# Kernel tuning notes

Hardware: AMD Instinct MI355X
Metric: run time of the kernel (lower is better)

The kernel has to match this reference:

```python
import jax, jax.numpy as jnp
import numpy as np

B, D, S = 8192, 512, 16
EPS = 1e-5


def setup_inputs() -> dict:
    key = jax.random.key(0)
    ks = jax.random.split(key, 12)
    w = lambda k, sh: (jax.random.normal(k, sh, dtype=jnp.float32) * 0.02)
    A_log = jnp.broadcast_to(jnp.log(jnp.arange(1, S + 1, dtype=jnp.float32)), (D, S))
    return {
        "x": jax.random.normal(ks[0], (B, D), dtype=jnp.float32),
        "ssm_state": jax.random.normal(ks[1], (B, D, S), dtype=jnp.float32) * 0.1,
        "ln_g": jnp.ones((D,), jnp.float32),
        "ln_b": jnp.zeros((D,), jnp.float32),
        "w1_W": w(ks[2], (D, D)), "w1_b": jnp.zeros((D,), jnp.float32),
        "v1_W": w(ks[3], (D, D)), "v1_b": jnp.zeros((D,), jnp.float32),
        "w2_W": w(ks[4], (D, D)), "w2_b": jnp.zeros((D,), jnp.float32),
        "conv_w": w(ks[5], (D, 1, 3)),  # depthwise Conv1d weight [C_out, 1, k]
        "A_log": A_log,
        "Bp_W": w(ks[6], (S, D)), "Bp_b": jnp.zeros((S,), jnp.float32),
        "Cp_W": w(ks[7], (S, D)), "Cp_b": jnp.zeros((S,), jnp.float32),
        "dt_W": w(ks[8], (D, D)), "dt_b": jnp.zeros((D,), jnp.float32),
    }


def reference(x, ssm_state, ln_g, ln_b, w1_W, w1_b, v1_W, v1_b, w2_W, w2_b,
              conv_w, A_log, Bp_W, Bp_b, Cp_W, Cp_b, dt_W, dt_b):
    # LayerNorm over d_model
    mu = jnp.mean(x, axis=-1, keepdims=True)
    var = jnp.mean(jnp.square(x - mu), axis=-1, keepdims=True)
    x_norm = (x - mu) * jax.lax.rsqrt(var + EPS) * ln_g + ln_b
    # w1 projection
    x1 = x_norm @ w1_W.T + w1_b
    # depthwise Conv1d on a length-1 sequence (unsqueeze(-1)): with k=3, pad=1,
    # zero padding means only the center tap contributes.
    x_conv = jax.nn.silu(x1 * conv_w[:, 0, 1])
    # selective-scan SSM single step (canonical Mamba recurrence)
    A = -jnp.exp(A_log)                                   # [D, S]
    delta = jax.nn.softplus(x_conv @ dt_W.T + dt_b)       # [B, D]
    Bm = x_conv @ Bp_W.T + Bp_b                           # [B, S]
    Cm = x_conv @ Cp_W.T + Cp_b                           # [B, S]
    dA = jnp.exp(delta[:, :, None] * A[None])             # [B, D, S]
    next_state = ssm_state * dA + (delta[:, :, None] * Bm[:, None, :]) * x_conv[:, :, None]
    x_ssm = jnp.sum(next_state * Cm[:, None, :], axis=-1)  # [B, D]
    # gate branch + output projection
    v = jax.nn.silu(x_norm @ v1_W.T + v1_b)
    out = (x_ssm * v) @ w2_W.T + w2_b
    return out, next_state
```

## Files before the change

### kernel.cpp

```cpp
#include <hip/hip_runtime.h>
#include <hip/hip_bf16.h>
#include <cstdint>
#include <cstddef>

#define Bn 8192
#define Dn 512
#define Sn 16

typedef __attribute__((ext_vector_type(4))) float f32x4;
typedef __attribute__((ext_vector_type(4))) unsigned int u32x4;
typedef __attribute__((ext_vector_type(8))) __bf16 bf16x8;
typedef __attribute__((ext_vector_type(8))) short short8;

union BF8 { short8 s; __hip_bfloat16 h[8]; };

__device__ __forceinline__ void gload16(const void* gsrc, void* ldst){
  __builtin_amdgcn_global_load_lds(
      (const __attribute__((address_space(1))) void*)gsrc,
      (__attribute__((address_space(3))) void*)ldst, 16, 0, 0);
}
__device__ __forceinline__ float bf2f(unsigned short u){
  union { unsigned int i; float f; } c; c.i = ((unsigned int)u) << 16; return c.f;
}
__device__ __forceinline__ unsigned short f2bfbits(float f){
  __hip_bfloat16 h = __float2bfloat16(f);
  return *(unsigned short*)&h;
}

__global__ __launch_bounds__(256) void prep_ln_kernel(
    const float* __restrict__ w1, const float* __restrict__ v1,
    const float* __restrict__ dt, const float* __restrict__ w2,
    const float* __restrict__ Bp, const float* __restrict__ Cp,
    const float* __restrict__ Alog,
    const float* __restrict__ x, const float* __restrict__ g,
    const float* __restrict__ bta,
    __hip_bfloat16* __restrict__ w1b, __hip_bfloat16* __restrict__ v1b,
    __hip_bfloat16* __restrict__ dtf, __hip_bfloat16* __restrict__ w2f,
    __hip_bfloat16* __restrict__ bpcpf, float* __restrict__ A,
    __hip_bfloat16* __restrict__ xn)
{
  const int bid = blockIdx.x;
  if(bid < Dn*Dn/256){
    const int i = bid*256 + threadIdx.x;
    w1b[i] = __float2bfloat16(w1[i]);
    v1b[i] = __float2bfloat16(v1[i]);
    const int t    = i >> 3, e = i & 7;
    const int lane = t & 63;
    const int kk   = (t >> 6) & 15;
    const int nt   = t >> 10;
    const int row  = nt*16 + (lane & 15);
    const int col  = kk*32 + (lane >> 4)*8 + e;
    dtf[i] = __float2bfloat16(dt[(size_t)row*Dn + col]);
    w2f[i] = __float2bfloat16(w2[(size_t)row*Dn + col]);
    if(i < 16384){
      const float src = (row < 16) ? Bp[(size_t)row*Dn + col]
                                   : Cp[(size_t)(row-16)*Dn + col];
      bpcpf[i] = __float2bfloat16(src);
    }
    if(i < Dn*Sn) A[i] = -expf(Alog[i]);
  } else {
    const int lane = threadIdx.x & 63;
    const int row  = (bid - Dn*Dn/256)*4 + (threadIdx.x >> 6);
    const float* xr = x + (size_t)row*Dn;
    const int c = lane*8;
    f32x4 a0 = *(const f32x4*)(xr + c);
    f32x4 a1 = *(const f32x4*)(xr + c + 4);
    float s = 0.f, q = 0.f;
    #pragma unroll
    for(int j=0;j<4;j++){ s += a0[j]+a1[j]; q += a0[j]*a0[j] + a1[j]*a1[j]; }
    #pragma unroll
    for(int off=32; off; off >>= 1){ s += __shfl_xor(s, off); q += __shfl_xor(q, off); }
    const float mu = s * (1.f/Dn);
    const float rs = rsqrtf(q*(1.f/Dn) - mu*mu + 1e-5f);
    f32x4 g0 = *(const f32x4*)(g + c);
    f32x4 g1 = *(const f32x4*)(g + c + 4);
    f32x4 b0 = *(const f32x4*)(bta + c);
    f32x4 b1 = *(const f32x4*)(bta + c + 4);
    BF8 o;
    #pragma unroll
    for(int j=0;j<4;j++){
      o.h[j]   = __float2bfloat16((a0[j]-mu)*rs*g0[j] + b0[j]);
      o.h[4+j] = __float2bfloat16((a1[j]-mu)*rs*g1[j] + b1[j]);
    }
    *(short8*)(xn + (size_t)row*Dn + c) = o.s;
  }
}

template<int ACT1, int ACT2, bool DUAL, bool OBF>
__global__ __launch_bounds__(256) void tgemm_kernel(
    const __hip_bfloat16* __restrict__ X,
    const __hip_bfloat16* __restrict__ W1,
    const __hip_bfloat16* __restrict__ W2,
    const float* __restrict__ bias1,
    const float* __restrict__ bias2,
    const float* __restrict__ convw,
    void* __restrict__ out1, void* __restrict__ out2,
    int M, int N, int K)
{
  constexpr int AB    = 8192;
  constexpr int B1B   = 4096;
  constexpr int BUFSZ = AB + B1B + (DUAL ? 4096 : 0);
  __shared__ char smem[3*BUFSZ] __attribute__((aligned(128)));

  const int tid  = threadIdx.x;
  const int wv   = tid >> 6;
  const int lane = tid & 63;

  const int r    = blockIdx.x + blockIdx.y*gridDim.x;
  const int qq   = (gridDim.x*gridDim.y) >> 3;
  const int o    = (r & 7)*qq + (r >> 3);
  const int tx   = o % gridDim.x;
  const int ty   = o / gridDim.x;
  const int r0 = ty * 128;
  const int c0 = tx * 64;

  f32x4 acc1[4][2] = {};
  f32x4 acc2[4][2] = {};

  const int lr = lane & 15;
  const int lg = lane >> 4;

  auto stage = [&](int buf, int kk){
    char* base = smem + buf*BUFSZ;
    #pragma unroll
    for(int i=0;i<2;i++){
      const int off = i*4096 + tid*16;
      const int row = off >> 6;
      const int g   = ((off>>4)&3) ^ ((row + (row>>3)) & 3);
      gload16(X + (size_t)(r0+row)*K + kk + g*8, base + i*4096 + (wv<<10));
    }
    {
      const int off = tid*16;
      const int row = off >> 6;
      const int g   = ((off>>4)&3) ^ ((row + (row>>3)) & 3);
      gload16(W1 + (size_t)(c0+row)*K + kk + g*8, base + AB + (wv<<10));
      if(DUAL)
        gload16(W2 + (size_t)(c0+row)*K + kk + g*8, base + AB + B1B + (wv<<10));
    }
  };

  const int NT = K >> 5;
  stage(0, 0);
  stage(1, 32);
  if constexpr (DUAL) asm volatile("s_waitcnt vmcnt(4)" ::: "memory");
  else                asm volatile("s_waitcnt vmcnt(3)" ::: "memory");
  __builtin_amdgcn_s_barrier();

  int cur = 0;
  for(int t=0; t<NT; ++t){
    if(t+2 < NT){
      int nb = cur + 2; if(nb >= 3) nb -= 3;
      stage(nb, (t+2)<<5);
    }

    const char* base = smem + cur*BUFSZ;
    bf16x8 af[4], b1f[2], b2f[2];
    #pragma unroll
    for(int m=0;m<4;m++){
      const int rr = (wv>>1)*64 + m*16 + lr;
      const int cc = lg ^ ((rr + (rr>>3)) & 3);
      af[m] = *(const bf16x8*)(base + rr*64 + cc*16);
    }
    #pragma unroll
    for(int n=0;n<2;n++){
      const int rr = (wv&1)*32 + n*16 + lr;
      const int cc = lg ^ ((rr + (rr>>3)) & 3);
      b1f[n] = *(const bf16x8*)(base + AB + rr*64 + cc*16);
      if(DUAL)
        b2f[n] = *(const bf16x8*)(base + AB + B1B + rr*64 + cc*16);
    }

    #pragma unroll
    for(int m=0;m<4;m++){
      #pragma unroll
      for(int n=0;n<2;n++){
        acc1[m][n] = __builtin_amdgcn_mfma_f32_16x16x32_bf16(af[m], b1f[n], acc1[m][n], 0, 0, 0);
        if(DUAL)
          acc2[m][n] = __builtin_amdgcn_mfma_f32_16x16x32_bf16(af[m], b2f[n], acc2[m][n], 0, 0, 0);
      }
    }

    if(t+1 < NT){
      if(t+2 < NT){
        if constexpr (DUAL) asm volatile("s_waitcnt vmcnt(4)" ::: "memory");
        else                asm volatile("s_waitcnt vmcnt(3)" ::: "memory");
      } else {
        asm volatile("s_waitcnt vmcnt(0)" ::: "memory");
      }
      __builtin_amdgcn_s_barrier();
    }
    cur += 1; if(cur == 3) cur = 0;
  }

  const int er = lg*4;
  const int ec = lr;
  #pragma unroll
  for(int n=0;n<2;n++){
    const int cc = c0 + (wv&1)*32 + n*16 + ec;
    const float bv1 = bias1[cc];
    const float cwv = (ACT1==1) ? convw[cc*3+1] : 0.f;
    const float bv2 = DUAL ? bias2[cc] : 0.f;
    #pragma unroll
    for(int m=0;m<4;m++){
      #pragma unroll
      for(int j=0;j<4;j++){
        const int rr = r0 + (wv>>1)*64 + m*16 + er + j;
        float y = acc1[m][n][j] + bv1;
        if(ACT1==1){ float z = y*cwv; y = z/(1.f + __expf(-z)); }
        if(ACT1==2){ y = y/(1.f + __expf(-y)); }
        if(ACT1==3){ y = (y > 20.f) ? y : log1pf(__expf(y)); }
        if(OBF) ((__hip_bfloat16*)out1)[(size_t)rr*N + cc] = __float2bfloat16(y);
        else    ((float*)out1)[(size_t)rr*N + cc] = y;
        if(DUAL){
          float y2 = acc2[m][n][j] + bv2;
          if(ACT2==1){ float z = y2*cwv; y2 = z/(1.f + __expf(-z)); }
          if(ACT2==2){ y2 = y2/(1.f + __expf(-y2)); }
          if(ACT2==3){ y2 = (y2 > 20.f) ? y2 : log1pf(__expf(y2)); }
          if(OBF) ((__hip_bfloat16*)out2)[(size_t)rr*N + cc] = __float2bfloat16(y2);
          else    ((float*)out2)[(size_t)rr*N + cc] = y2;
        }
      }
    }
  }
}

__global__ __launch_bounds__(512) void mega_kernel(
    const __hip_bfloat16* __restrict__ xconv,
    const __hip_bfloat16* __restrict__ vbuf,
    const __hip_bfloat16* __restrict__ dtf,
    const __hip_bfloat16* __restrict__ bpcpf,
    const __hip_bfloat16* __restrict__ w2f,
    const float* __restrict__ dt_b,
    const float* __restrict__ bpb,
    const float* __restrict__ cpb,
    const float* __restrict__ w2_b,
    const float* __restrict__ A,
    const float* __restrict__ state,
    float* __restrict__ nstate,
    float* __restrict__ out)
{
  __shared__ char xcs[16*1024];
  __shared__ char dls[16*1024];
  __shared__ char vls[16*1024];
  __shared__ float bc[16][32];

  const int b    = blockIdx.x;
  const int tid  = threadIdx.x;
  const int wv   = tid >> 6;
  const int lane = tid & 63;
  const int lr   = lane & 15;
  const int lg   = lane >> 4;
  const size_t row0 = (size_t)b * 16;

  const int squad = tid & 3;
  const int slot  = tid >> 2;

  #pragma unroll
  for(int p2=0;p2<2;p2++){
    const int e   = p2*4096 + tid*8;
    const int row = e >> 9;
    const int col = e & 511;
    const int sw  = row*1024 + (((col>>3) ^ (row&7))<<4);
    *(u32x4*)(xcs + sw) = *(const u32x4*)(xconv + row0*Dn + e);
    *(u32x4*)(vls + sw) = *(const u32x4*)(vbuf  + row0*Dn + e);
  }

  const f32x4 Av = *(const f32x4*)(A + squad*4);
  f32x4 st[4], stn[4];
  {
    const size_t base0 = (row0*Dn)*Sn + squad*4;
    #pragma unroll
    for(int pp=0;pp<4;pp++){
      st[pp]  = *(const f32x4*)(state + base0 + (size_t)(pp*128+slot)*Sn);
      stn[pp] = *(const f32x4*)(state + base0 + (size_t)Dn*Sn + (size_t)(pp*128+slot)*Sn);
    }
  }
  __syncthreads();

  #pragma unroll 1
  for(int ti=0; ti<5; ++ti){
    int nt;
    if(ti < 4) nt = wv + ti*8;
    else { if(wv >= 2) break; nt = 32 + wv; }
    const __hip_bfloat16* Bf = (nt < 32)
        ? (dtf   + ((size_t)nt*16)*512)
        : (bpcpf + ((size_t)(nt-32)*16)*512);
    f32x4 acc = {};
    #pragma unroll
    for(int kk=0; kk<16; ++kk){
      bf16x8 a  = *(const bf16x8*)(xcs + lr*1024 + ((((kk*4+lg)) ^ (lr&7))<<4));
      bf16x8 bv = *(const bf16x8*)(Bf + (size_t)kk*512 + lane*8);
      acc = __builtin_amdgcn_mfma_f32_16x16x32_bf16(a, bv, acc, 0, 0, 0);
    }
    if(nt < 32){
      const int col = nt*16 + lr;
      const float bvs = dt_b[col];
      #pragma unroll
      for(int j=0;j<4;j++){
        const int row = lg*4 + j;
        float y = acc[j] + bvs;
        y = (y > 20.f) ? y : log1pf(__expf(y));
        *(unsigned short*)(dls + row*1024 + (((col>>3) ^ (row&7))<<4) + (col&7)*2)
            = f2bfbits(y);
      }
    } else {
      const float bvs = (nt==32) ? bpb[lr] : cpb[lr];
      #pragma unroll
      for(int j=0;j<4;j++){
        const int row = lg*4 + j;
        bc[row][(nt-32)*16 + lr] = acc[j] + bvs;
      }
    }
  }
  __syncthreads();

  #pragma unroll 1
  for(int rr=0; rr<16; ++rr){
    const size_t base = ((row0 + rr)*Dn)*Sn + squad*4;
    f32x4 stn2[4];
    if(rr < 14){
      const size_t base2 = base + (size_t)2*Dn*Sn;
      #pragma unroll
      for(int pp=0;pp<4;pp++)
        stn2[pp] = *(const f32x4*)(state + base2 + (size_t)(pp*128+slot)*Sn);
    }
    const f32x4 bm = *(const f32x4*)&bc[rr][squad*4];
    const f32x4 cm = *(const f32x4*)&bc[rr][16 + squad*4];
    #pragma unroll
    for(int pp=0;pp<4;pp++){
      const int d = pp*128 + slot;
      const int la = rr*1024 + (((d>>3) ^ (rr&7))<<4) + (d&7)*2;
      const float dl = bf2f(*(const unsigned short*)(dls + la));
      const float xc = bf2f(*(const unsigned short*)(xcs + la));
      f32x4 ns;
      float xs = 0.f;
      #pragma unroll
      for(int j=0;j<4;j++){
        const float da = __expf(dl * Av[j]);
        const float nv = st[pp][j]*da + dl*bm[j]*xc;
        ns[j] = nv;
        xs += nv * cm[j];
      }
      __builtin_nontemporal_store(ns, (f32x4*)(nstate + base + (size_t)d*Sn));
      xs += __shfl_xor(xs, 1);
      xs += __shfl_xor(xs, 2);
      if(squad == 0){
        const float vv = bf2f(*(const unsigned short*)(vls + la));
        *(unsigned short*)(xcs + la) = f2bfbits(xs * vv);
      }
    }
    #pragma unroll
    for(int pp=0;pp<4;pp++){ st[pp] = stn[pp]; stn[pp] = stn2[pp]; }
  }
  __syncthreads();

  #pragma unroll 1
  for(int ti=0; ti<4; ++ti){
    const int nt = wv + ti*8;
    const __hip_bfloat16* Bf = w2f + ((size_t)nt*16)*512;
    f32x4 acc = {};
    #pragma unroll
    for(int kk=0; kk<16; ++kk){
      bf16x8 a  = *(const bf16x8*)(xcs + lr*1024 + ((((kk*4+lg)) ^ (lr&7))<<4));
      bf16x8 bv = *(const bf16x8*)(Bf + (size_t)kk*512 + lane*8);
      acc = __builtin_amdgcn_mfma_f32_16x16x32_bf16(a, bv, acc, 0, 0, 0);
    }
    const int col = nt*16 + lr;
    const float bvs = w2_b[col];
    #pragma unroll
    for(int j=0;j<4;j++){
      const int row = lg*4 + j;
      out[(row0 + row)*Dn + col] = acc[j] + bvs;
    }
  }
}

extern "C" void kernel_launch(void* const* d_in, const int* in_sizes, int n_in,
                              void* d_out, int out_size, void* d_ws, size_t ws_size,
                              hipStream_t stream)
{
  const float* x      = (const float*)d_in[0];
  const float* sst    = (const float*)d_in[1];
  const float* ln_g   = (const float*)d_in[2];
  const float* ln_b   = (const float*)d_in[3];
  const float* w1_W   = (const float*)d_in[4];
  const float* w1_b   = (const float*)d_in[5];
  const float* v1_W   = (const float*)d_in[6];
  const float* v1_b   = (const float*)d_in[7];
  const float* w2_W   = (const float*)d_in[8];
  const float* w2_b   = (const float*)d_in[9];
  const float* conv_w = (const float*)d_in[10];
  const float* A_log  = (const float*)d_in[11];
  const float* Bp_W   = (const float*)d_in[12];
  const float* Bp_b   = (const float*)d_in[13];
  const float* Cp_W   = (const float*)d_in[14];
  const float* Cp_b   = (const float*)d_in[15];
  const float* dt_W   = (const float*)d_in[16];
  const float* dt_b   = (const float*)d_in[17];

  float* out    = (float*)d_out;
  float* nstate = out + (size_t)Bn*Dn;

  char* wsp = (char*)d_ws;
  auto alloc = [&](size_t bytes)->char*{
    char* p = wsp; wsp += (bytes + 255) & ~(size_t)255; return p;
  };
  __hip_bfloat16* xnorm = (__hip_bfloat16*)alloc((size_t)Bn*Dn*2);
  __hip_bfloat16* xconv = (__hip_bfloat16*)alloc((size_t)Bn*Dn*2);
  __hip_bfloat16* vbuf  = (__hip_bfloat16*)alloc((size_t)Bn*Dn*2);
  __hip_bfloat16* w1b   = (__hip_bfloat16*)alloc((size_t)Dn*Dn*2);
  __hip_bfloat16* v1b   = (__hip_bfloat16*)alloc((size_t)Dn*Dn*2);
  __hip_bfloat16* dtf   = (__hip_bfloat16*)alloc((size_t)Dn*Dn*2);
  __hip_bfloat16* w2f   = (__hip_bfloat16*)alloc((size_t)Dn*Dn*2);
  __hip_bfloat16* bpcpf = (__hip_bfloat16*)alloc((size_t)2*Sn*Dn*2);
  float*          Abuf  = (float*)alloc((size_t)Dn*Sn*4);

  prep_ln_kernel<<<dim3(Dn*Dn/256 + Bn/4), dim3(256), 0, stream>>>(
      w1_W, v1_W, dt_W, w2_W, Bp_W, Cp_W, A_log, x, ln_g, ln_b,
      w1b, v1b, dtf, w2f, bpcpf, Abuf, xnorm);
  tgemm_kernel<1,2,true,true><<<dim3(Dn/64, Bn/128), dim3(256), 0, stream>>>(
      xnorm, w1b, v1b, w1_b, v1_b, conv_w, (void*)xconv, (void*)vbuf, Bn, Dn, Dn);
  mega_kernel<<<dim3(Bn/16), dim3(512), 0, stream>>>(
      xconv, vbuf, dtf, bpcpf, w2f, dt_b, Bp_b, Cp_b, w2_b, Abuf,
      sst, nstate, out);
}
```

Before: 165.9 us.

## Split mega kernel across two D-halves with atomic-add output projection

Doubles the mega_kernel grid so each block handles half of the D dimension: its delta GEMM columns, its state slice, and a K-split partial of the w2 projection. The partial outputs are combined with float atomic adds into an output buffer that the prep kernel pre-fills with the w2 bias. This is meant to raise parallelism and occupancy (fewer registers and less LDS per block). The cost is that every output element now takes two atomic adds, summation order becomes nondeterministic, and the B/C projections are computed twice, once per half.

Result: faster. 161.8 us (median of 2 runs) (-2.4%).

```diff
diff --git a/kernel.cpp b/kernel.cpp
--- a/kernel.cpp
+++ b/kernel.cpp
@@ -33,11 +33,11 @@
     const float* __restrict__ Bp, const float* __restrict__ Cp,
     const float* __restrict__ Alog,
     const float* __restrict__ x, const float* __restrict__ g,
-    const float* __restrict__ bta,
+    const float* __restrict__ bta, const float* __restrict__ w2bias,
     __hip_bfloat16* __restrict__ w1b, __hip_bfloat16* __restrict__ v1b,
     __hip_bfloat16* __restrict__ dtf, __hip_bfloat16* __restrict__ w2f,
     __hip_bfloat16* __restrict__ bpcpf, float* __restrict__ A,
-    __hip_bfloat16* __restrict__ xn)
+    __hip_bfloat16* __restrict__ xn, float* __restrict__ outp)
 {
   const int bid = blockIdx.x;
   if(bid < Dn*Dn/256){
@@ -83,6 +83,8 @@
       o.h[4+j] = __float2bfloat16((a1[j]-mu)*rs*g1[j] + b1[j]);
     }
     *(short8*)(xn + (size_t)row*Dn + c) = o.s;
+    *(f32x4*)(outp + (size_t)row*Dn + c)     = *(const f32x4*)(w2bias + c);
+    *(f32x4*)(outp + (size_t)row*Dn + c + 4) = *(const f32x4*)(w2bias + c + 4);
   }
 }
 
@@ -233,18 +235,19 @@
     const float* __restrict__ dt_b,
     const float* __restrict__ bpb,
     const float* __restrict__ cpb,
-    const float* __restrict__ w2_b,
     const float* __restrict__ A,
     const float* __restrict__ state,
     float* __restrict__ nstate,
     float* __restrict__ out)
 {
   __shared__ char xcs[16*1024];
-  __shared__ char dls[16*1024];
-  __shared__ char vls[16*1024];
+  __shared__ char dls[16*512];
+  __shared__ char vls[16*512];
   __shared__ float bc[16][32];
 
-  const int b    = blockIdx.x;
+  const int b     = blockIdx.x & 511;
+  const int dhalf = blockIdx.x >> 9;
+  const int dh256 = dhalf*256;
   const int tid  = threadIdx.x;
   const int wv   = tid >> 6;
   const int lane = tid & 63;
@@ -260,17 +263,23 @@
     const int e   = p2*4096 + tid*8;
     const int row = e >> 9;
     const int col = e & 511;
-    const int sw  = row*1024 + (((col>>3) ^ (row&7))<<4);
-    *(u32x4*)(xcs + sw) = *(const u32x4*)(xconv + row0*Dn + e);
-    *(u32x4*)(vls + sw) = *(const u32x4*)(vbuf  + row0*Dn + e);
+    *(u32x4*)(xcs + row*1024 + (((col>>3) ^ (row&7))<<4)) =
+        *(const u32x4*)(xconv + row0*Dn + e);
+  }
+  {
+    const int e   = tid*8;
+    const int row = e >> 8;
+    const int col = e & 255;
+    *(u32x4*)(vls + row*512 + (((col>>3) ^ (row&7))<<4)) =
+        *(const u32x4*)(vbuf + (row0+row)*Dn + dh256 + col);
   }
 
   const f32x4 Av = *(const f32x4*)(A + squad*4);
-  f32x4 st[4], stn[4];
+  f32x4 st[2], stn[2];
   {
-    const size_t base0 = (row0*Dn)*Sn + squad*4;
-    #pragma unroll
-    for(int pp=0;pp<4;pp++){
+    const size_t base0 = (row0*Dn + dh256)*Sn + squad*4;
+    #pragma unroll
+    for(int pp=0;pp<2;pp++){
       st[pp]  = *(const f32x4*)(state + base0 + (size_t)(pp*128+slot)*Sn);
       stn[pp] = *(const f32x4*)(state + base0 + (size_t)Dn*Sn + (size_t)(pp*128+slot)*Sn);
     }
@@ -278,13 +287,11 @@
   __syncthreads();
 
   #pragma unroll 1
-  for(int ti=0; ti<5; ++ti){
-    int nt;
-    if(ti < 4) nt = wv + ti*8;
-    else { if(wv >= 2) break; nt = 32 + wv; }
-    const __hip_bfloat16* Bf = (nt < 32)
-        ? (dtf   + ((size_t)nt*16)*512)
-        : (bpcpf + ((size_t)(nt-32)*16)*512);
+  for(int ti=0; ti<3; ++ti){
+    int ntl;
+    const __hip_bfloat16* Bf;
+    if(ti < 2){ ntl = wv + ti*8; Bf = dtf + ((size_t)(dh256/16 + ntl)*16)*512; }
+    else { if(wv >= 2) break; ntl = 16 + wv; Bf = bpcpf + ((size_t)wv*16)*512; }
     f32x4 acc = {};
     #pragma unroll
     for(int kk=0; kk<16; ++kk){
@@ -292,23 +299,23 @@
       bf16x8 bv = *(const bf16x8*)(Bf + (size_t)kk*512 + lane*8);
       acc = __builtin_amdgcn_mfma_f32_16x16x32_bf16(a, bv, acc, 0, 0, 0);
     }
-    if(nt < 32){
-      const int col = nt*16 + lr;
-      const float bvs = dt_b[col];
+    if(ntl < 16){
+      const int coll = ntl*16 + lr;
+      const float bvs = dt_b[dh256 + coll];
       #pragma unroll
       for(int j=0;j<4;j++){
         const int row = lg*4 + j;
         float y = acc[j] + bvs;
         y = (y > 20.f) ? y : log1pf(__expf(y));
-        *(unsigned short*)(dls + row*1024 + (((col>>3) ^ (row&7))<<4) + (col&7)*2)
+        *(unsigned short*)(dls + row*512 + (((coll>>3) ^ (row&7))<<4) + (coll&7)*2)
             = f2bfbits(y);
       }
     } else {
-      const float bvs = (nt==32) ? bpb[lr] : cpb[lr];
+      const float bvs = (ntl==16) ? bpb[lr] : cpb[lr];
       #pragma unroll
       for(int j=0;j<4;j++){
         const int row = lg*4 + j;
-        bc[row][(nt-32)*16 + lr] = acc[j] + bvs;
+        bc[row][(ntl-16)*16 + lr] = acc[j] + bvs;
       }
     }
   }
@@ -316,22 +323,24 @@
 
   #pragma unroll 1
   for(int rr=0; rr<16; ++rr){
-    const size_t base = ((row0 + rr)*Dn)*Sn + squad*4;
-    f32x4 stn2[4];
+    const size_t base = ((row0 + rr)*Dn + dh256)*Sn + squad*4;
+    f32x4 stn2[2];
     if(rr < 14){
       const size_t base2 = base + (size_t)2*Dn*Sn;
       #pragma unroll
-      for(int pp=0;pp<4;pp++)
+      for(int pp=0;pp<2;pp++)
         stn2[pp] = *(const f32x4*)(state + base2 + (size_t)(pp*128+slot)*Sn);
     }
     const f32x4 bm = *(const f32x4*)&bc[rr][squad*4];
     const f32x4 cm = *(const f32x4*)&bc[rr][16 + squad*4];
     #pragma unroll
-    for(int pp=0;pp<4;pp++){
-      const int d = pp*128 + slot;
-      const int la = rr*1024 + (((d>>3) ^ (rr&7))<<4) + (d&7)*2;
-      const float dl = bf2f(*(const unsigned short*)(dls + la));
-      const float xc = bf2f(*(const unsigned short*)(xcs + la));
+    for(int pp=0;pp<2;pp++){
+      const int dl_ = pp*128 + slot;
+      const int dg  = dh256 + dl_;
+      const int lah = rr*512  + (((dl_>>3) ^ (rr&7))<<4) + (dl_&7)*2;
+      const int laf = rr*1024 + (((dg >>3) ^ (rr&7))<<4) + (dg &7)*2;
+      const float dl = bf2f(*(const unsigned short*)(dls + lah));
+      const float xc = bf2f(*(const unsigned short*)(xcs + laf));
       f32x4 ns;
       float xs = 0.f;
       #pragma unroll
@@ -341,36 +350,35 @@
         ns[j] = nv;
         xs += nv * cm[j];
       }
-      __builtin_nontemporal_store(ns, (f32x4*)(nstate + base + (size_t)d*Sn));
+      __builtin_nontemporal_store(ns, (f32x4*)(nstate + base + (size_t)dl_*Sn));
       xs += __shfl_xor(xs, 1);
       xs += __shfl_xor(xs, 2);
       if(squad == 0){
-        const float vv = bf2f(*(const unsigned short*)(vls + la));
-        *(unsigned short*)(xcs + la) = f2bfbits(xs * vv);
-      }
-    }
-    #pragma unroll
-    for(int pp=0;pp<4;pp++){ st[pp] = stn[pp]; stn[pp] = stn2[pp]; }
+        const float vv = bf2f(*(const unsigned short*)(vls + lah));
+        *(unsigned short*)(xcs + laf) = f2bfbits(xs * vv);
+      }
+    }
+    #pragma unroll
+    for(int pp=0;pp<2;pp++){ st[pp] = stn[pp]; stn[pp] = stn2[pp]; }
   }
   __syncthreads();
 
   #pragma unroll 1
   for(int ti=0; ti<4; ++ti){
     const int nt = wv + ti*8;
-    const __hip_bfloat16* Bf = w2f + ((size_t)nt*16)*512;
     f32x4 acc = {};
     #pragma unroll
-    for(int kk=0; kk<16; ++kk){
-      bf16x8 a  = *(const bf16x8*)(xcs + lr*1024 + ((((kk*4+lg)) ^ (lr&7))<<4));
-      bf16x8 bv = *(const bf16x8*)(Bf + (size_t)kk*512 + lane*8);
+    for(int kkl=0; kkl<8; ++kkl){
+      const int kkg = dhalf*8 + kkl;
+      bf16x8 a  = *(const bf16x8*)(xcs + lr*1024 + ((((kkg*4+lg)) ^ (lr&7))<<4));
+      bf16x8 bv = *(const bf16x8*)(w2f + ((size_t)(nt*16 + kkg))*512 + lane*8);
       acc = __builtin_amdgcn_mfma_f32_16x16x32_bf16(a, bv, acc, 0, 0, 0);
     }
     const int col = nt*16 + lr;
-    const float bvs = w2_b[col];
     #pragma unroll
     for(int j=0;j<4;j++){
       const int row = lg*4 + j;
-      out[(row0 + row)*Dn + col] = acc[j] + bvs;
+      unsafeAtomicAdd(&out[(row0 + row)*Dn + col], acc[j]);
     }
   }
 }
@@ -416,11 +424,11 @@
   float*          Abuf  = (float*)alloc((size_t)Dn*Sn*4);
 
   prep_ln_kernel<<<dim3(Dn*Dn/256 + Bn/4), dim3(256), 0, stream>>>(
-      w1_W, v1_W, dt_W, w2_W, Bp_W, Cp_W, A_log, x, ln_g, ln_b,
-      w1b, v1b, dtf, w2f, bpcpf, Abuf, xnorm);
+      w1_W, v1_W, dt_W, w2_W, Bp_W, Cp_W, A_log, x, ln_g, ln_b, w2_b,
+      w1b, v1b, dtf, w2f, bpcpf, Abuf, xnorm, out);
   tgemm_kernel<1,2,true,true><<<dim3(Dn/64, Bn/128), dim3(256), 0, stream>>>(
       xnorm, w1b, v1b, w1_b, v1_b, conv_w, (void*)xconv, (void*)vbuf, Bn, Dn, Dn);
-  mega_kernel<<<dim3(Bn/16), dim3(512), 0, stream>>>(
-      xconv, vbuf, dtf, bpcpf, w2f, dt_b, Bp_b, Cp_b, w2_b, Abuf,
+  mega_kernel<<<dim3(Bn/16*2), dim3(512), 0, stream>>>(
+      xconv, vbuf, dtf, bpcpf, w2f, dt_b, Bp_b, Cp_b, Abuf,
       sst, nstate, out);
 }
```

## Fuse w1/v1 GEMMs into mega kernel, dropping separate tiled GEMM launch

Applied to the files above, without the earlier changes.

Removes the standalone tiled GEMM that wrote xconv and v to global memory. The mega kernel now loads the normalized input tile into LDS and computes the w1 and v1 projections per 16-row block with MFMA, reading weights pre-swizzled into fragment layout. This saves a kernel launch and the write and read-back of two B×D bf16 intermediates. In exchange each block re-reads the full w1 and v1 weights from global/L2 with no LDS tiling reuse and does more serial work per block, and LDS is reused between the projections and delta.

Result: slower. 208.1 us (+25.5%).

```diff
diff --git a/kernel.cpp b/kernel.cpp
--- a/kernel.cpp
+++ b/kernel.cpp
@@ -14,11 +14,6 @@
 
 union BF8 { short8 s; __hip_bfloat16 h[8]; };
 
-__device__ __forceinline__ void gload16(const void* gsrc, void* ldst){
-  __builtin_amdgcn_global_load_lds(
-      (const __attribute__((address_space(1))) void*)gsrc,
-      (__attribute__((address_space(3))) void*)ldst, 16, 0, 0);
-}
 __device__ __forceinline__ float bf2f(unsigned short u){
   union { unsigned int i; float f; } c; c.i = ((unsigned int)u) << 16; return c.f;
 }
@@ -34,7 +29,7 @@
     const float* __restrict__ Alog,
     const float* __restrict__ x, const float* __restrict__ g,
     const float* __restrict__ bta,
-    __hip_bfloat16* __restrict__ w1b, __hip_bfloat16* __restrict__ v1b,
+    __hip_bfloat16* __restrict__ w1f, __hip_bfloat16* __restrict__ v1f,
     __hip_bfloat16* __restrict__ dtf, __hip_bfloat16* __restrict__ w2f,
     __hip_bfloat16* __restrict__ bpcpf, float* __restrict__ A,
     __hip_bfloat16* __restrict__ xn)
@@ -42,19 +37,19 @@
   const int bid = blockIdx.x;
   if(bid < Dn*Dn/256){
     const int i = bid*256 + threadIdx.x;
-    w1b[i] = __float2bfloat16(w1[i]);
-    v1b[i] = __float2bfloat16(v1[i]);
     const int t    = i >> 3, e = i & 7;
     const int lane = t & 63;
     const int kk   = (t >> 6) & 15;
     const int nt   = t >> 10;
     const int row  = nt*16 + (lane & 15);
     const int col  = kk*32 + (lane >> 4)*8 + e;
-    dtf[i] = __float2bfloat16(dt[(size_t)row*Dn + col]);
-    w2f[i] = __float2bfloat16(w2[(size_t)row*Dn + col]);
+    const size_t s = (size_t)row*Dn + col;
+    w1f[i] = __float2bfloat16(w1[s]);
+    v1f[i] = __float2bfloat16(v1[s]);
+    dtf[i] = __float2bfloat16(dt[s]);
+    w2f[i] = __float2bfloat16(w2[s]);
     if(i < 16384){
-      const float src = (row < 16) ? Bp[(size_t)row*Dn + col]
-                                   : Cp[(size_t)(row-16)*Dn + col];
+      const float src = (row < 16) ? Bp[s] : Cp[(size_t)(row-16)*Dn + col];
       bpcpf[i] = __float2bfloat16(src);
     }
     if(i < Dn*Sn) A[i] = -expf(Alog[i]);
@@ -86,150 +81,16 @@
   }
 }
 
-template<int ACT1, int ACT2, bool DUAL, bool OBF>
-__global__ __launch_bounds__(256) void tgemm_kernel(
-    const __hip_bfloat16* __restrict__ X,
-    const __hip_bfloat16* __restrict__ W1,
-    const __hip_bfloat16* __restrict__ W2,
-    const float* __restrict__ bias1,
-    const float* __restrict__ bias2,
-    const float* __restrict__ convw,
-    void* __restrict__ out1, void* __restrict__ out2,
-    int M, int N, int K)
-{
-  constexpr int AB    = 8192;
-  constexpr int B1B   = 4096;
-  constexpr int BUFSZ = AB + B1B + (DUAL ? 4096 : 0);
-  __shared__ char smem[3*BUFSZ] __attribute__((aligned(128)));
-
-  const int tid  = threadIdx.x;
-  const int wv   = tid >> 6;
-  const int lane = tid & 63;
-
-  const int r    = blockIdx.x + blockIdx.y*gridDim.x;
-  const int qq   = (gridDim.x*gridDim.y) >> 3;
-  const int o    = (r & 7)*qq + (r >> 3);
-  const int tx   = o % gridDim.x;
-  const int ty   = o / gridDim.x;
-  const int r0 = ty * 128;
-  const int c0 = tx * 64;
-
-  f32x4 acc1[4][2] = {};
-  f32x4 acc2[4][2] = {};
-
-  const int lr = lane & 15;
-  const int lg = lane >> 4;
-
-  auto stage = [&](int buf, int kk){
-    char* base = smem + buf*BUFSZ;
-    #pragma unroll
-    for(int i=0;i<2;i++){
-      const int off = i*4096 + tid*16;
-      const int row = off >> 6;
-      const int g   = ((off>>4)&3) ^ ((row + (row>>3)) & 3);
-      gload16(X + (size_t)(r0+row)*K + kk + g*8, base + i*4096 + (wv<<10));
-    }
-    {
-      const int off = tid*16;
-      const int row = off >> 6;
-      const int g   = ((off>>4)&3) ^ ((row + (row>>3)) & 3);
-      gload16(W1 + (size_t)(c0+row)*K + kk + g*8, base + AB + (wv<<10));
-      if(DUAL)
-        gload16(W2 + (size_t)(c0+row)*K + kk + g*8, base + AB + B1B + (wv<<10));
-    }
-  };
-
-  const int NT = K >> 5;
-  stage(0, 0);
-  stage(1, 32);
-  if constexpr (DUAL) asm volatile("s_waitcnt vmcnt(4)" ::: "memory");
-  else                asm volatile("s_waitcnt vmcnt(3)" ::: "memory");
-  __builtin_amdgcn_s_barrier();
-
-  int cur = 0;
-  for(int t=0; t<NT; ++t){
-    if(t+2 < NT){
-      int nb = cur + 2; if(nb >= 3) nb -= 3;
-      stage(nb, (t+2)<<5);
-    }
-
-    const char* base = smem + cur*BUFSZ;
-    bf16x8 af[4], b1f[2], b2f[2];
-    #pragma unroll
-    for(int m=0;m<4;m++){
-      const int rr = (wv>>1)*64 + m*16 + lr;
-      const int cc = lg ^ ((rr + (rr>>3)) & 3);
-      af[m] = *(const bf16x8*)(base + rr*64 + cc*16);
-    }
-    #pragma unroll
-    for(int n=0;n<2;n++){
-      const int rr = (wv&1)*32 + n*16 + lr;
-      const int cc = lg ^ ((rr + (rr>>3)) & 3);
-      b1f[n] = *(const bf16x8*)(base + AB + rr*64 + cc*16);
-      if(DUAL)
-        b2f[n] = *(const bf16x8*)(base + AB + B1B + rr*64 + cc*16);
-    }
-
-    #pragma unroll
-    for(int m=0;m<4;m++){
-      #pragma unroll
-      for(int n=0;n<2;n++){
-        acc1[m][n] = __builtin_amdgcn_mfma_f32_16x16x32_bf16(af[m], b1f[n], acc1[m][n], 0, 0, 0);
-        if(DUAL)
-          acc2[m][n] = __builtin_amdgcn_mfma_f32_16x16x32_bf16(af[m], b2f[n], acc2[m][n], 0, 0, 0);
-      }
-    }
-
-    if(t+1 < NT){
-      if(t+2 < NT){
-        if constexpr (DUAL) asm volatile("s_waitcnt vmcnt(4)" ::: "memory");
-        else                asm volatile("s_waitcnt vmcnt(3)" ::: "memory");
-      } else {
-        asm volatile("s_waitcnt vmcnt(0)" ::: "memory");
-      }
-      __builtin_amdgcn_s_barrier();
-    }
-    cur += 1; if(cur == 3) cur = 0;
-  }
-
-  const int er = lg*4;
-  const int ec = lr;
-  #pragma unroll
-  for(int n=0;n<2;n++){
-    const int cc = c0 + (wv&1)*32 + n*16 + ec;
-    const float bv1 = bias1[cc];
-    const float cwv = (ACT1==1) ? convw[cc*3+1] : 0.f;
-    const float bv2 = DUAL ? bias2[cc] : 0.f;
-    #pragma unroll
-    for(int m=0;m<4;m++){
-      #pragma unroll
-      for(int j=0;j<4;j++){
-        const int rr = r0 + (wv>>1)*64 + m*16 + er + j;
-        float y = acc1[m][n][j] + bv1;
-        if(ACT1==1){ float z = y*cwv; y = z/(1.f + __expf(-z)); }
-        if(ACT1==2){ y = y/(1.f + __expf(-y)); }
-        if(ACT1==3){ y = (y > 20.f) ? y : log1pf(__expf(y)); }
-        if(OBF) ((__hip_bfloat16*)out1)[(size_t)rr*N + cc] = __float2bfloat16(y);
-        else    ((float*)out1)[(size_t)rr*N + cc] = y;
-        if(DUAL){
-          float y2 = acc2[m][n][j] + bv2;
-          if(ACT2==1){ float z = y2*cwv; y2 = z/(1.f + __expf(-z)); }
-          if(ACT2==2){ y2 = y2/(1.f + __expf(-y2)); }
-          if(ACT2==3){ y2 = (y2 > 20.f) ? y2 : log1pf(__expf(y2)); }
-          if(OBF) ((__hip_bfloat16*)out2)[(size_t)rr*N + cc] = __float2bfloat16(y2);
-          else    ((float*)out2)[(size_t)rr*N + cc] = y2;
-        }
-      }
-    }
-  }
-}
-
 __global__ __launch_bounds__(512) void mega_kernel(
-    const __hip_bfloat16* __restrict__ xconv,
-    const __hip_bfloat16* __restrict__ vbuf,
+    const __hip_bfloat16* __restrict__ xn,
+    const __hip_bfloat16* __restrict__ w1f,
+    const __hip_bfloat16* __restrict__ v1f,
     const __hip_bfloat16* __restrict__ dtf,
     const __hip_bfloat16* __restrict__ bpcpf,
     const __hip_bfloat16* __restrict__ w2f,
+    const float* __restrict__ w1_b,
+    const float* __restrict__ v1_b,
+    const float* __restrict__ convw,
     const float* __restrict__ dt_b,
     const float* __restrict__ bpb,
     const float* __restrict__ cpb,
@@ -239,8 +100,8 @@
     float* __restrict__ nstate,
     float* __restrict__ out)
 {
+  __shared__ char bufA[16*1024];
   __shared__ char xcs[16*1024];
-  __shared__ char dls[16*1024];
   __shared__ char vls[16*1024];
   __shared__ float bc[16][32];
 
@@ -260,9 +121,8 @@
     const int e   = p2*4096 + tid*8;
     const int row = e >> 9;
     const int col = e & 511;
-    const int sw  = row*1024 + (((col>>3) ^ (row&7))<<4);
-    *(u32x4*)(xcs + sw) = *(const u32x4*)(xconv + row0*Dn + e);
-    *(u32x4*)(vls + sw) = *(const u32x4*)(vbuf  + row0*Dn + e);
+    *(u32x4*)(bufA + row*1024 + (((col>>3) ^ (row&7))<<4)) =
+        *(const u32x4*)(xn + row0*Dn + e);
   }
 
   const f32x4 Av = *(const f32x4*)(A + squad*4);
@@ -273,6 +133,44 @@
     for(int pp=0;pp<4;pp++){
       st[pp]  = *(const f32x4*)(state + base0 + (size_t)(pp*128+slot)*Sn);
       stn[pp] = *(const f32x4*)(state + base0 + (size_t)Dn*Sn + (size_t)(pp*128+slot)*Sn);
+    }
+  }
+  __syncthreads();
+
+  #pragma unroll 1
+  for(int ti=0; ti<8; ++ti){
+    const bool isX = (ti < 4);
+    const int nt = wv + (isX ? ti : ti-4)*8;
+    const __hip_bfloat16* Bf = (isX ? w1f : v1f) + ((size_t)nt*16)*512;
+    f32x4 acc = {};
+    #pragma unroll
+    for(int kk=0; kk<16; ++kk){
+      bf16x8 a  = *(const bf16x8*)(bufA + lr*1024 + ((((kk*4+lg)) ^ (lr&7))<<4));
+      bf16x8 bv = *(const bf16x8*)(Bf + (size_t)kk*512 + lane*8);
+      acc = __builtin_amdgcn_mfma_f32_16x16x32_bf16(a, bv, acc, 0, 0, 0);
+    }
+    const int col = nt*16 + lr;
+    if(isX){
+      const float bvs = w1_b[col];
+      const float cwv = convw[col*3+1];
+      #pragma unroll
+      for(int j=0;j<4;j++){
+        const int row = lg*4 + j;
+        float z = (acc[j] + bvs) * cwv;
+        z = z/(1.f + __expf(-z));
+        *(unsigned short*)(xcs + row*1024 + (((col>>3) ^ (row&7))<<4) + (col&7)*2)
+            = f2bfbits(z);
+      }
+    } else {
+      const float bvs = v1_b[col];
+      #pragma unroll
+      for(int j=0;j<4;j++){
+        const int row = lg*4 + j;
+        float y = acc[j] + bvs;
+        y = y/(1.f + __expf(-y));
+        *(unsigned short*)(vls + row*1024 + (((col>>3) ^ (row&7))<<4) + (col&7)*2)
+            = f2bfbits(y);
+      }
     }
   }
   __syncthreads();
@@ -300,7 +198,7 @@
         const int row = lg*4 + j;
         float y = acc[j] + bvs;
         y = (y > 20.f) ? y : log1pf(__expf(y));
-        *(unsigned short*)(dls + row*1024 + (((col>>3) ^ (row&7))<<4) + (col&7)*2)
+        *(unsigned short*)(bufA + row*1024 + (((col>>3) ^ (row&7))<<4) + (col&7)*2)
             = f2bfbits(y);
       }
     } else {
@@ -330,7 +228,7 @@
     for(int pp=0;pp<4;pp++){
       const int d = pp*128 + slot;
       const int la = rr*1024 + (((d>>3) ^ (rr&7))<<4) + (d&7)*2;
-      const float dl = bf2f(*(const unsigned short*)(dls + la));
+      const float dl = bf2f(*(const unsigned short*)(bufA + la));
       const float xc = bf2f(*(const unsigned short*)(xcs + la));
       f32x4 ns;
       float xs = 0.f;
@@ -406,10 +304,8 @@
     char* p = wsp; wsp += (bytes + 255) & ~(size_t)255; return p;
   };
   __hip_bfloat16* xnorm = (__hip_bfloat16*)alloc((size_t)Bn*Dn*2);
-  __hip_bfloat16* xconv = (__hip_bfloat16*)alloc((size_t)Bn*Dn*2);
-  __hip_bfloat16* vbuf  = (__hip_bfloat16*)alloc((size_t)Bn*Dn*2);
-  __hip_bfloat16* w1b   = (__hip_bfloat16*)alloc((size_t)Dn*Dn*2);
-  __hip_bfloat16* v1b   = (__hip_bfloat16*)alloc((size_t)Dn*Dn*2);
+  __hip_bfloat16* w1f   = (__hip_bfloat16*)alloc((size_t)Dn*Dn*2);
+  __hip_bfloat16* v1f   = (__hip_bfloat16*)alloc((size_t)Dn*Dn*2);
   __hip_bfloat16* dtf   = (__hip_bfloat16*)alloc((size_t)Dn*Dn*2);
   __hip_bfloat16* w2f   = (__hip_bfloat16*)alloc((size_t)Dn*Dn*2);
   __hip_bfloat16* bpcpf = (__hip_bfloat16*)alloc((size_t)2*Sn*Dn*2);
@@ -417,10 +313,8 @@
 
   prep_ln_kernel<<<dim3(Dn*Dn/256 + Bn/4), dim3(256), 0, stream>>>(
       w1_W, v1_W, dt_W, w2_W, Bp_W, Cp_W, A_log, x, ln_g, ln_b,
-      w1b, v1b, dtf, w2f, bpcpf, Abuf, xnorm);
-  tgemm_kernel<1,2,true,true><<<dim3(Dn/64, Bn/128), dim3(256), 0, stream>>>(
-      xnorm, w1b, v1b, w1_b, v1_b, conv_w, (void*)xconv, (void*)vbuf, Bn, Dn, Dn);
+      w1f, v1f, dtf, w2f, bpcpf, Abuf, xnorm);
   mega_kernel<<<dim3(Bn/16), dim3(512), 0, stream>>>(
-      xconv, vbuf, dtf, bpcpf, w2f, dt_b, Bp_b, Cp_b, w2_b, Abuf,
-      sst, nstate, out);
-}
+      xnorm, w1f, v1f, dtf, bpcpf, w2f, w1_b, v1_b, conv_w,
+      dt_b, Bp_b, Cp_b, w2_b, Abuf, sst, nstate, out);
+}
```
